# Optimization experiments

Hardware: AMD Instinct MI355X
Metric: run time of the kernel (lower is better)

Reference implementation:

```python
import jax, jax.numpy as jnp
import numpy as np

B, N, OUTERDIM, DIM, N_CLASSES = 2, 6000, 1024, 512, 2
HEADS, DIM_HEAD, INNER = 8, 64, 512
LANDMARKS, PINV_ITERS, KPAD = 256, 6, 16  # residual conv kernel 33 -> pad 16
SCALE = DIM_HEAD ** -0.5


def layer_norm(x, g, b, eps=1e-5):
    mu = x.mean(-1, keepdims=True)
    var = jnp.var(x, axis=-1, keepdims=True)
    return (x - mu) * jax.lax.rsqrt(var + eps) * g + b


def moore_penrose_pinv(x, iters=PINV_ITERS):
    # x: [b, h, m, m]
    abs_x = jnp.abs(x)
    col = abs_x.sum(-1)
    row = abs_x.sum(-2)
    z = jnp.swapaxes(x, -1, -2) / (jnp.max(col) * jnp.max(row))
    I = jnp.eye(x.shape[-1], dtype=x.dtype)
    for _ in range(iters):
        xz = x @ z
        z = 0.25 * z @ (13 * I - xz @ (15 * I - xz @ (7 * I - xz)))
    return z


def nystrom_attention(x, w_qkv, w_out, b_out, conv_w):
    b, n, _ = x.shape
    pad = (-n) % LANDMARKS
    xp = jnp.pad(x, ((0, 0), (pad, 0), (0, 0)))  # pad at FRONT, as in lucidrains impl
    npad = n + pad
    qkv = xp @ w_qkv.T  # [b, npad, 3*inner]
    q, k, v = [t.reshape(b, npad, HEADS, DIM_HEAD).transpose(0, 2, 1, 3)
               for t in jnp.split(qkv, 3, axis=-1)]
    q = q * SCALE
    l = npad // LANDMARKS  # tokens per landmark
    q_l = q.reshape(b, HEADS, LANDMARKS, l, DIM_HEAD).sum(3) / l
    k_l = k.reshape(b, HEADS, LANDMARKS, l, DIM_HEAD).sum(3) / l
    attn1 = jax.nn.softmax(jnp.einsum('bhid,bhjd->bhij', q, k_l), axis=-1)   # [b,h,npad,m]
    attn2 = jax.nn.softmax(jnp.einsum('bhid,bhjd->bhij', q_l, k_l), axis=-1)  # [b,h,m,m]
    attn3 = jax.nn.softmax(jnp.einsum('bhid,bhjd->bhij', q_l, k), axis=-1)    # [b,h,m,npad]
    out = (attn1 @ moore_penrose_pinv(attn2)) @ (attn3 @ v)  # [b,h,npad,d]
    # depthwise residual conv over sequence dim (per head), kernel (33,1)
    out = out + jax.lax.conv_general_dilated(
        v, conv_w, window_strides=(1, 1), padding=((KPAD, KPAD), (0, 0)),
        dimension_numbers=('NCHW', 'OIHW', 'NCHW'), feature_group_count=HEADS)
    out = out.transpose(0, 2, 1, 3).reshape(b, npad, INNER)
    out = out @ w_out.T + b_out
    return out[:, -n:]


def setup_inputs() -> dict:
    key = jax.random.key(0)
    ks = jax.random.split(key, 12)
    w = lambda k, shape: 0.02 * jax.random.normal(k, shape, dtype=jnp.float32)
    inp = {
        'data': jax.random.normal(ks[0], (B, N, OUTERDIM), dtype=jnp.float32),
        'w1': w(ks[1], (DIM, OUTERDIM)), 'b1': jnp.zeros((DIM,), jnp.float32),
        'cls_token': jax.random.normal(ks[2], (1, 1, DIM), dtype=jnp.float32),
        'ln1_g': jnp.ones((DIM,), jnp.float32), 'ln1_b': jnp.zeros((DIM,), jnp.float32),
        'qkv1_w': w(ks[3], (3 * INNER, DIM)),
        'out1_w': w(ks[4], (DIM, INNER)), 'out1_b': jnp.zeros((DIM,), jnp.float32),
        'conv1_w': w(ks[5], (HEADS, 1, 33, 1)),
        'ln2_g': jnp.ones((DIM,), jnp.float32), 'ln2_b': jnp.zeros((DIM,), jnp.float32),
        'qkv2_w': w(ks[6], (3 * INNER, DIM)),
        'out2_w': w(ks[7], (DIM, INNER)), 'out2_b': jnp.zeros((DIM,), jnp.float32),
        'conv2_w': w(ks[8], (HEADS, 1, 33, 1)),
        'lnf_g': jnp.ones((DIM,), jnp.float32), 'lnf_b': jnp.zeros((DIM,), jnp.float32),
        'w2': w(ks[9], (N_CLASSES, DIM)), 'b2': jnp.zeros((N_CLASSES,), jnp.float32),
    }
    return inp


def reference(data, w1, b1, cls_token, ln1_g, ln1_b, qkv1_w, out1_w, out1_b, conv1_w,
              ln2_g, ln2_b, qkv2_w, out2_w, out2_b, conv2_w, lnf_g, lnf_b, w2, b2):
    h = jax.nn.relu(data @ w1.T + b1)  # [B, N, DIM]
    H = h.shape[1]
    side = int(np.ceil(np.sqrt(H)))
    add = side * side - H
    h = jnp.concatenate([h, h[:, :add]], axis=1)  # square padding: 6084
    cls = jnp.broadcast_to(cls_token, (h.shape[0], 1, h.shape[2]))
    h = jnp.concatenate([cls, h], axis=1)  # +CLS: 6085
    h = h + nystrom_attention(layer_norm(h, ln1_g, ln1_b), qkv1_w, out1_w, out1_b, conv1_w)
    h = h + nystrom_attention(layer_norm(h, ln2_g, ln2_b), qkv2_w, out2_w, out2_b, conv2_w)
    h = layer_norm(h, lnf_g, lnf_b)[:, 0]
    logits = h @ w2.T + b2
    return logits
```

## Files before the change

### kernel.cpp

```cpp
#include <hip/hip_runtime.h>
#include <cstdint>
#include <cstddef>

namespace {

constexpr int DIMC  = 512;
constexpr int SEQ   = 6085;
constexpr int NPAD  = 6144;
constexpr int PADF  = 59;
constexpr int LMK   = 256;
constexpr int BHN   = 16;
constexpr int KSPL  = 16;
constexpr int MPADR = 6016;

typedef __attribute__((ext_vector_type(8))) short bf8_t;
typedef __attribute__((ext_vector_type(4))) float f4_t;

#define MFMA(a, b, c) __builtin_amdgcn_mfma_f32_16x16x32_bf16(a, b, c, 0, 0, 0)

#define SWZB(r, cu) (((((r) << 6) + ((cu) << 1))) ^ (((r) & 7) << 4))

#define GLDS16(gp, lp) __builtin_amdgcn_global_load_lds( \
    (const __attribute__((address_space(1))) void*)(gp), \
    (__attribute__((address_space(3))) void*)(lp), 16, 0, 0)

__device__ __forceinline__ ushort f2bf(float f) {
    union { float f; uint32_t u; } c{f};
    uint32_t u = c.u;
    return (ushort)((u + 0x7FFFu + ((u >> 16) & 1u)) >> 16);
}
__device__ __forceinline__ float bf2f(ushort u) {
    union { uint32_t u; float f; } c{(uint32_t)u << 16};
    return c.f;
}

__device__ __forceinline__ float waveSum(float v) {
#pragma unroll
    for (int o = 32; o > 0; o >>= 1) v += __shfl_xor(v, o, 64);
    return v;
}
__device__ __forceinline__ float waveMax(float v) {
#pragma unroll
    for (int o = 32; o > 0; o >>= 1) v = fmaxf(v, __shfl_xor(v, o, 64));
    return v;
}
__device__ __forceinline__ float blockSum256(float v, float* sm) {
    v = waveSum(v);
    __syncthreads();
    if ((threadIdx.x & 63) == 0) sm[threadIdx.x >> 6] = v;
    __syncthreads();
    return sm[0] + sm[1] + sm[2] + sm[3];
}
__device__ __forceinline__ float blockMax256(float v, float* sm) {
    v = waveMax(v);
    __syncthreads();
    if ((threadIdx.x & 63) == 0) sm[threadIdx.x >> 6] = v;
    __syncthreads();
    return fmaxf(fmaxf(sm[0], sm[1]), fmaxf(sm[2], sm[3]));
}
__device__ __forceinline__ float grpMax(float v) {
    v = fmaxf(v, __shfl_xor(v, 1, 64));
    v = fmaxf(v, __shfl_xor(v, 2, 64));
    v = fmaxf(v, __shfl_xor(v, 4, 64));
    v = fmaxf(v, __shfl_xor(v, 8, 64));
    return v;
}
__device__ __forceinline__ float grpSum(float v) {
    v += __shfl_xor(v, 1, 64);
    v += __shfl_xor(v, 2, 64);
    v += __shfl_xor(v, 4, 64);
    v += __shfl_xor(v, 8, 64);
    return v;
}

template<int EPI>
__global__ __launch_bounds__(256)
void gemm_bt(const ushort* __restrict__ A, const ushort* __restrict__ B,
             void* __restrict__ Cv, int M, int N, int K,
             int lda, int ldb, int ldc,
             long long sA, long long sB, long long sC,
             const float* __restrict__ bias, int relu,
             ushort* __restrict__ qp, ushort* __restrict__ kp, ushort* __restrict__ vp)
{
    __shared__ __align__(16) char As_s[128 * 128];
    __shared__ __align__(16) char Bs_s[128 * 128];
    const int gx = gridDim.x, gy = gridDim.y;
    const int total = gx * gy * gridDim.z;
    int flat = (blockIdx.z * gy + blockIdx.y) * gx + blockIdx.x;
    {
        int q = total >> 3, r = total & 7;
        int xcd = flat & 7, idx = flat >> 3;
        flat = (xcd < r ? xcd * (q + 1) : r * (q + 1) + (xcd - r) * q) + idx;
    }
    const int z = flat / (gx * gy);
    const int rem = flat - z * gx * gy;
    const int by = rem / gx, bx = rem - by * gx;

    const ushort* Ab = A + (size_t)z * sA;
    const ushort* Bb = B + (size_t)z * sB;
    const int row0 = by * 128, col0 = bx * 128;
    const int tid = threadIdx.x, wid = tid >> 6, lane = tid & 63;
    const int wr = wid >> 1, wc = wid & 1, lr = lane & 15, kg = lane >> 4;
    const int srow = lane >> 3, sq = lane & 7;
    f4_t acc[4][4] = {};
    for (int k0 = 0; k0 < K; k0 += 64) {
        __syncthreads();
#pragma unroll
        for (int i = 0; i < 4; ++i) {
            int r = wid * 32 + i * 8 + srow;
            int qs = sq ^ (r & 7);
            GLDS16(Ab + (size_t)(row0 + r) * lda + k0 + qs * 8,
                   As_s + (wid * 32 + i * 8) * 128);
        }
#pragma unroll
        for (int i = 0; i < 4; ++i) {
            int r = wid * 32 + i * 8 + srow;
            int qs = sq ^ (r & 7);
            GLDS16(Bb + (size_t)(col0 + r) * ldb + k0 + qs * 8,
                   Bs_s + (wid * 32 + i * 8) * 128);
        }
        asm volatile("s_waitcnt vmcnt(0)" ::: "memory");
        __syncthreads();
#pragma unroll
        for (int ks = 0; ks < 2; ++ks) {
            bf8_t af[4], bg[4];
#pragma unroll
            for (int mr = 0; mr < 4; ++mr) {
                int r = wr * 64 + mr * 16 + lr;
                af[mr] = *(const bf8_t*)(As_s + r * 128 + ((((ks << 2) | kg) ^ (r & 7)) << 4));
            }
#pragma unroll
            for (int nr = 0; nr < 4; ++nr) {
                int r = wc * 64 + nr * 16 + lr;
                bg[nr] = *(const bf8_t*)(Bs_s + r * 128 + ((((ks << 2) | kg) ^ (r & 7)) << 4));
            }
#pragma unroll
            for (int mr = 0; mr < 4; ++mr)
#pragma unroll
                for (int nr = 0; nr < 4; ++nr)
                    acc[mr][nr] = MFMA(af[mr], bg[nr], acc[mr][nr]);
        }
    }
#pragma unroll
    for (int mr = 0; mr < 4; ++mr) {
#pragma unroll
        for (int nr = 0; nr < 4; ++nr) {
#pragma unroll
            for (int r = 0; r < 4; ++r) {
                int gm = row0 + wr * 64 + mr * 16 + kg * 4 + r;
                int gn = col0 + wc * 64 + nr * 16 + lr;
                if (gm >= M || gn >= N) continue;
                float val = acc[mr][nr][r];
                if (EPI == 0) {
                    if (bias) val += bias[gn];
                    if (relu) val = fmaxf(val, 0.f);
                    ((float*)Cv)[(size_t)z * sC + (size_t)gm * ldc + gn] = val;
                } else if (EPI == 1) {
                    ((ushort*)Cv)[(size_t)z * sC + (size_t)gm * ldc + gn] = f2bf(val);
                } else {
                    int b = (gm >= NPAD) ? 1 : 0;
                    int i = gm - b * NPAD;
                    int which = gn >> 9, hh = (gn >> 6) & 7, d = gn & 63;
                    int bh = b * 8 + hh;
                    if (which == 0)
                        qp[((size_t)bh * NPAD + i) * 64 + d] = f2bf(val * 0.125f);
                    else if (which == 1)
                        kp[((size_t)bh * NPAD + i) * 64 + d] = f2bf(val);
                    else
                        vp[((size_t)bh * NPAD + i) * 64 + d] = f2bf(val);
                }
            }
        }
    }
}

template<int OC, int OCT, int CTD>
__global__ __launch_bounds__(256)
void gemm_nt(const ushort* __restrict__ A, const ushort* __restrict__ Bt,
             ushort* __restrict__ C, ushort* __restrict__ CT,
             float alpha, float cd, int K, int ldC, int ldCT,
             long long sA, long long sBt, long long sC, long long sCT)
{
    __shared__ __align__(16) char As_s[64 * 64];
    __shared__ __align__(16) char Bs_s[64 * 64];
    const int z = blockIdx.z;
    const int row0 = blockIdx.y * 64, col0 = blockIdx.x * 64;
    const int tid = threadIdx.x, wid = tid >> 6, lane = tid & 63;
    const int lr = lane & 15, kg = lane >> 4;
    const ushort* Ab = A + (size_t)z * sA;
    const ushort* Bb = Bt + (size_t)z * sBt;
    const int sr = tid >> 2, sc = (tid & 3) * 8;
    f4_t acc[4] = {};
    for (int k0 = 0; k0 < K; k0 += 32) {
        *(bf8_t*)(As_s + SWZB(sr, sc)) = *(const bf8_t*)&Ab[(size_t)(row0 + sr) * K + k0 + sc];
        *(bf8_t*)(Bs_s + SWZB(sr, sc)) = *(const bf8_t*)&Bb[(size_t)(col0 + sr) * K + k0 + sc];
        __syncthreads();
        bf8_t af = *(const bf8_t*)(As_s + SWZB(wid * 16 + lr, kg * 8));
#pragma unroll
        for (int j = 0; j < 4; ++j) {
            bf8_t bg = *(const bf8_t*)(Bs_s + SWZB(j * 16 + lr, kg * 8));
            acc[j] = MFMA(af, bg, acc[j]);
        }
        __syncthreads();
    }
#pragma unroll
    for (int j = 0; j < 4; ++j) {
#pragma unroll
        for (int r = 0; r < 4; ++r) {
            int gm = row0 + wid * 16 + kg * 4 + r;
            int gn = col0 + j * 16 + lr;
            float val = alpha * acc[j][r];
            if (OC) C[(size_t)z * sC + (size_t)gm * ldC + gn] = f2bf(val);
            if (OCT) CT[(size_t)z * sCT + (size_t)gn * ldCT + gm] =
                f2bf(CTD ? (((gm == gn) ? cd : 0.f) - val) : val);
        }
    }
}

__global__ __launch_bounds__(256)
void pv_splitk(const ushort* __restrict__ S, const ushort* __restrict__ v,
               float* __restrict__ o2p)
{
    __shared__ __align__(16) char As_s[128 * 64];
    __shared__ __align__(16) char Bs_s[64 * 64];
    const int split = blockIdx.x, mt = blockIdx.y, bh = blockIdx.z;
    const int tid = threadIdx.x;
    const int wid = tid >> 6, lane = tid & 63;
    const int lr = lane & 15, kg = lane >> 4;
    const ushort* Sb = S + (size_t)bh * LMK * NPAD + (size_t)(mt * 128) * NPAD;
    const ushort* vb = v + (size_t)bh * NPAD * 64;
    const int ks0 = split * (NPAD / KSPL);
    f4_t acc[2][4] = {};
    for (int k0 = ks0; k0 < ks0 + NPAD / KSPL; k0 += 32) {
#pragma unroll
        for (int p = 0; p < 2; ++p) {
            int idx = p * 256 + tid;
            int m = idx >> 2, kc = (idx & 3) * 8;
            *(bf8_t*)(As_s + SWZB(m, kc)) = *(const bf8_t*)&Sb[(size_t)m * NPAD + k0 + kc];
        }
#pragma unroll
        for (int p = 0; p < 8; ++p) {
            int kk = p * 4 + (tid >> 6), n = tid & 63;
            *(ushort*)(Bs_s + SWZB(n, kk)) = vb[(size_t)(k0 + kk) * 64 + n];
        }
        __syncthreads();
        bf8_t af[2], bg[4];
#pragma unroll
        for (int i = 0; i < 2; ++i)
            af[i] = *(const bf8_t*)(As_s + SWZB(wid * 32 + i * 16 + lr, kg * 8));
#pragma unroll
        for (int j = 0; j < 4; ++j)
            bg[j] = *(const bf8_t*)(Bs_s + SWZB(j * 16 + lr, kg * 8));
#pragma unroll
        for (int i = 0; i < 2; ++i)
#pragma unroll
            for (int j = 0; j < 4; ++j)
                acc[i][j] = MFMA(af[i], bg[j], acc[i][j]);
        __syncthreads();
    }
#pragma unroll
    for (int i = 0; i < 2; ++i)
#pragma unroll
        for (int j = 0; j < 4; ++j)
#pragma unroll
            for (int r = 0; r < 4; ++r) {
                int gm = mt * 128 + wid * 32 + i * 16 + kg * 4 + r;
                int gn = j * 16 + lr;
                o2p[((size_t)(split * BHN + bh) * LMK + gm) * 64 + gn] = acc[i][j][r];
            }
}

__global__ void reduce_o2(const float* __restrict__ o2p, ushort* __restrict__ o2t) {
    int idx = blockIdx.x * 256 + threadIdx.x;
    int bh = idx >> 14, m = (idx >> 6) & 255, d = idx & 63;
    float s = 0.f;
#pragma unroll
    for (int sp = 0; sp < KSPL; ++sp)
        s += o2p[((size_t)(sp * BHN + bh) << 14) + (m << 6) + d];
    o2t[((size_t)bh * 64 + d) * 256 + m] = f2bf(s);
}

__global__ __launch_bounds__(256)
void attn1_fused(const ushort* __restrict__ q, const ushort* __restrict__ kl,
                 const ushort* __restrict__ Wt, ushort* __restrict__ ot)
{
    __shared__ __align__(16) char P_s[64 * 512];
    const int mt = blockIdx.x;
    const int bh = blockIdx.y;
    const int b = bh >> 3, hh = bh & 7;
    const int tid = threadIdx.x, wid = tid >> 6, lane = tid & 63;
    const int lr = lane & 15, kg = lane >> 4;
    const int row0 = mt * 64, rowb = wid * 16;
    const ushort* qb  = q  + (size_t)bh * NPAD * 64;
    const ushort* klb = kl + (size_t)bh * LMK * 64;
    const ushort* Wtb = Wt + (size_t)bh * 128 * 256;

    f4_t acc[16];
#pragma unroll
    for (int nf = 0; nf < 16; ++nf) acc[nf] = (f4_t){0.f, 0.f, 0.f, 0.f};
#pragma unroll
    for (int ks = 0; ks < 2; ++ks) {
        bf8_t af = *(const bf8_t*)&qb[(size_t)(row0 + rowb + lr) * 64 + ks * 32 + kg * 8];
#pragma unroll
        for (int nf = 0; nf < 16; ++nf) {
            bf8_t bg = *(const bf8_t*)&klb[(size_t)(nf * 16 + lr) * 64 + ks * 32 + kg * 8];
            acc[nf] = MFMA(af, bg, acc[nf]);
        }
    }
    float inv_s[4];
    {
        float mx[4] = {-3.0e38f, -3.0e38f, -3.0e38f, -3.0e38f};
#pragma unroll
        for (int nf = 0; nf < 16; ++nf)
#pragma unroll
            for (int r = 0; r < 4; ++r) mx[r] = fmaxf(mx[r], acc[nf][r]);
#pragma unroll
        for (int r = 0; r < 4; ++r) mx[r] = grpMax(mx[r]);
        float sum[4] = {0.f, 0.f, 0.f, 0.f};
        const int rb2 = rowb + kg * 4;
        const int cc2 = (lr & 7) * 2, chi = lr >> 3;
#pragma unroll
        for (int nf = 0; nf < 16; ++nf)
#pragma unroll
            for (int r = 0; r < 4; ++r) {
                float e = __expf(acc[nf][r] - mx[r]);
                sum[r] += e;
                int row = rb2 + r;
                int chunk = (2 * nf + chi) ^ (row & 7);
                *(ushort*)(P_s + row * 512 + chunk * 16 + cc2) = f2bf(e);
            }
#pragma unroll
        for (int r = 0; r < 4; ++r) inv_s[r] = 1.f / grpSum(sum[r]);
    }
    f4_t acc2[4] = {};
#pragma unroll
    for (int kt = 0; kt < 8; ++kt) {
        int row = rowb + lr;
        int chunk = (kt * 4 + kg) ^ (row & 7);
        bf8_t af2 = *(const bf8_t*)(P_s + row * 512 + chunk * 16);
#pragma unroll
        for (int nf = 0; nf < 4; ++nf) {
            bf8_t bg = *(const bf8_t*)&Wtb[(size_t)(nf * 16 + lr) * 256 + kt * 32 + kg * 8];
            acc2[nf] = MFMA(af2, bg, acc2[nf]);
        }
    }
#pragma unroll
    for (int nf = 0; nf < 4; ++nf)
#pragma unroll
        for (int r = 0; r < 4; ++r) {
            int gm = row0 + rowb + kg * 4 + r;
            int gn = nf * 16 + lr;
            ot[((size_t)(b * NPAD + gm)) * DIMC + hh * 64 + gn] = f2bf(acc2[nf][r] * inv_s[r]);
        }
}

__global__ void cvt_bf16(const float* __restrict__ in, ushort* __restrict__ out, int n8) {
    int i = blockIdx.x * 256 + threadIdx.x;
    if (i >= n8) return;
    float4 a = ((const float4*)in)[i * 2], b = ((const float4*)in)[i * 2 + 1];
    ushort4 lo = { f2bf(a.x), f2bf(a.y), f2bf(a.z), f2bf(a.w) };
    ushort4 hi = { f2bf(b.x), f2bf(b.y), f2bf(b.z), f2bf(b.w) };
    ((ushort4*)out)[i * 2] = lo;
    ((ushort4*)out)[i * 2 + 1] = hi;
}

__global__ void extend_h(float* __restrict__ h, const float* __restrict__ cls) {
    int b = blockIdx.y, bx = blockIdx.x;
    float* hb = h + (size_t)b * SEQ * DIMC;
    for (int c = threadIdx.x; c < DIMC; c += 256) {
        if (bx == 0) hb[c] = cls[c];
        else hb[(size_t)(6000 + bx) * DIMC + c] = hb[(size_t)bx * DIMC + c];
    }
}

__global__ void zero_xp_pad(ushort* __restrict__ xp) {
    int e = blockIdx.x * 256 + threadIdx.x;
    int b = e / (PADF * DIMC);
    int rest = e - b * (PADF * DIMC);
    xp[(size_t)b * NPAD * DIMC + rest] = 0;
}

__global__ __launch_bounds__(128)
void ln_to_xp(const float* __restrict__ h, const float* __restrict__ g,
              const float* __restrict__ bb, ushort* __restrict__ xp)
{
    __shared__ float sm[2];
    int r = blockIdx.x;
    int b = r / SEQ, i = r - b * SEQ;
    int t = threadIdx.x;
    const float4* row = (const float4*)(h + (size_t)r * DIMC);
    float4 x = row[t];
    float s  = x.x + x.y + x.z + x.w;
    float sq = x.x * x.x + x.y * x.y + x.z * x.z + x.w * x.w;
    s = waveSum(s);
    sq = waveSum(sq);
    int w = t >> 6;
    if ((t & 63) == 0) sm[w] = s;
    __syncthreads();
    float S = sm[0] + sm[1];
    __syncthreads();
    if ((t & 63) == 0) sm[w] = sq;
    __syncthreads();
    float SQ = sm[0] + sm[1];
    float mu = S * (1.f / DIMC);
    float var = SQ * (1.f / DIMC) - mu * mu;
    float rs = rsqrtf(var + 1e-5f);
    float4 gg = ((const float4*)g)[t];
    float4 bv = ((const float4*)bb)[t];
    ushort4 o;
    o.x = f2bf((x.x - mu) * rs * gg.x + bv.x);
    o.y = f2bf((x.y - mu) * rs * gg.y + bv.y);
    o.z = f2bf((x.z - mu) * rs * gg.z + bv.z);
    o.w = f2bf((x.w - mu) * rs * gg.w + bv.w);
    ((ushort4*)(xp + ((size_t)b * NPAD + PADF + i) * DIMC))[t] = o;
}

__global__ void landmark_mean(const ushort* __restrict__ in, ushort* __restrict__ out) {
    int m = blockIdx.x, bh = blockIdx.y, d = threadIdx.x;
    const ushort* p = in + ((size_t)bh * NPAD + (size_t)m * (NPAD / LMK)) * 64 + d;
    float s = 0.f;
#pragma unroll
    for (int j = 0; j < NPAD / LMK; ++j) s += bf2f(p[(size_t)j * 64]);
    out[((size_t)bh * LMK + m) * 64 + d] = f2bf(s * (1.f / (NPAD / LMK)));
}

__global__ __launch_bounds__(256)
void softmax_bf_wide(ushort* __restrict__ S) {
    __shared__ float sm[4];
    ushort* p = S + (size_t)blockIdx.x * NPAD;
    int t = threadIdx.x;
    float v[24];
    float mx = -1e30f;
#pragma unroll
    for (int j = 0; j < 24; ++j) { v[j] = bf2f(p[j * 256 + t]); mx = fmaxf(mx, v[j]); }
    float bm = blockMax256(mx, sm);
    float s = 0.f;
#pragma unroll
    for (int j = 0; j < 24; ++j) { v[j] = __expf(v[j] - bm); s += v[j]; }
    float bs = blockSum256(s, sm);
    float inv = 1.f / bs;
#pragma unroll
    for (int j = 0; j < 24; ++j) p[j * 256 + t] = f2bf(v[j] * inv);
}

__global__ __launch_bounds__(256)
void softmax_bf256(ushort* __restrict__ S) {
    __shared__ float sm[4];
    ushort* p = S + (size_t)blockIdx.x * 256;
    int t = threadIdx.x;
    float v = bf2f(p[t]);
    float bm = blockMax256(v, sm);
    float e = __expf(v - bm);
    float bs = blockSum256(e, sm);
    p[t] = f2bf(e / bs);
}

__global__ __launch_bounds__(256)
void colsum_max(const ushort* __restrict__ X, float* __restrict__ scal) {
    __shared__ float sm[4];
    int bh = blockIdx.x, t = threadIdx.x;
    const ushort* Xb = X + ((size_t)bh << 16);
    float s = 0.f;
#pragma unroll 8
    for (int i = 0; i < 256; ++i) s += bf2f(Xb[(size_t)i * 256 + t]);
    float m = blockMax256(s, sm);
    if (t == 0) atomicMax((unsigned int*)scal, __float_as_uint(m));
}

__global__ void init_z(const ushort* __restrict__ X, const float* __restrict__ scal,
                       ushort* __restrict__ Z, ushort* __restrict__ Zt) {
    size_t e = (size_t)blockIdx.x * 256 + threadIdx.x;
    int c = (int)(e & 255);
    int r = (int)((e >> 8) & 255);
    size_t bh = e >> 16;
    float inv = 1.f / scal[0];
    Z[e]  = f2bf(bf2f(X[(bh << 16) + (size_t)c * 256 + r]) * inv);
    Zt[e] = f2bf(bf2f(X[e]) * inv);
}

__global__ __launch_bounds__(256)
void conv_add(const ushort* __restrict__ v, const float* __restrict__ cw,
              ushort* __restrict__ ot)
{
    __shared__ float w[33];
    __shared__ ushort vt[96][64];
    int bh = blockIdx.y;
    int b = bh >> 3, hh = bh & 7;
    int i0 = blockIdx.x * 64;
    int t = threadIdx.x;
    if (t < 33) w[t] = cw[hh * 33 + t];
    const ushort* vb = v + (size_t)bh * NPAD * 64;
    int d = t & 63;
    for (int rr = t >> 6; rr < 96; rr += 4) {
        int j = i0 - 16 + rr;
        vt[rr][d] = (j >= 0 && j < NPAD) ? vb[(size_t)j * 64 + d] : (ushort)0;
    }
    __syncthreads();
    for (int ii = t >> 6; ii < 64; ii += 4) {
        float acc = 0.f;
#pragma unroll
        for (int kk = 0; kk < 33; ++kk) acc += w[kk] * bf2f(vt[ii + kk][d]);
        size_t off = ((size_t)(b * NPAD + i0 + ii)) * DIMC + hh * 64 + d;
        ot[off] = f2bf(bf2f(ot[off]) + acc);
    }
}

__global__ void residual_add(float* __restrict__ h, const float* __restrict__ y) {
    size_t e = (size_t)blockIdx.x * 256 + threadIdx.x;
    int c = (int)(e & 511);
    size_t ri = e >> 9;
    int i = (int)(ri % SEQ);
    int b = (int)(ri / SEQ);
    h[e] += y[((size_t)b * NPAD + PADF + i) * DIMC + c];
}

__global__ __launch_bounds__(256)
void final_head(const float* __restrict__ h, const float* __restrict__ g,
                const float* __restrict__ bb, const float* __restrict__ w2,
                const float* __restrict__ b2, float* __restrict__ out)
{
    __shared__ float row[DIMC];
    __shared__ float sm[4];
    int b = blockIdx.x;
    int t = threadIdx.x;
    const float* x = h + (size_t)b * SEQ * DIMC;
    float v0 = x[t], v1 = x[t + 256];
    float S = blockSum256(v0 + v1, sm);
    float SQ = blockSum256(v0 * v0 + v1 * v1, sm);
    float mu = S * (1.f / DIMC);
    float rs = rsqrtf(SQ * (1.f / DIMC) - mu * mu + 1e-5f);
    row[t] = (v0 - mu) * rs * g[t] + bb[t];
    row[t + 256] = (v1 - mu) * rs * g[t + 256] + bb[t + 256];
    __syncthreads();
    if (t < 64) {
        float a0 = 0.f, a1 = 0.f;
        for (int idx = t; idx < DIMC; idx += 64) {
            a0 += row[idx] * w2[idx];
            a1 += row[idx] * w2[DIMC + idx];
        }
        a0 = waveSum(a0);
        a1 = waveSum(a1);
        if (t == 0) {
            out[b * 2 + 0] = a0 + b2[0];
            out[b * 2 + 1] = a1 + b2[1];
        }
    }
}

void bt(int epi, const ushort* A, const ushort* B, void* C, int M, int N, int K,
        int lda, int ldb, int ldc, long long sA, long long sB, long long sC, int batch,
        const float* bias, int relu, ushort* qp, ushort* kp, ushort* vp, hipStream_t s)
{
    dim3 g((N + 127) / 128, (M + 127) / 128, batch), blk(256);
    switch (epi) {
    case 0: gemm_bt<0><<<g, blk, 0, s>>>(A, B, C, M, N, K, lda, ldb, ldc, sA, sB, sC, bias, relu, qp, kp, vp); break;
    case 1: gemm_bt<1><<<g, blk, 0, s>>>(A, B, C, M, N, K, lda, ldb, ldc, sA, sB, sC, bias, relu, qp, kp, vp); break;
    default: gemm_bt<2><<<g, blk, 0, s>>>(A, B, C, M, N, K, lda, ldb, ldc, sA, sB, sC, bias, relu, qp, kp, vp); break;
    }
}

void nt(int mode, const ushort* A, const ushort* Bt, ushort* C, ushort* CT,
        float alpha, float cd, int M, int N, int K, int ldC, int ldCT,
        long long sA, long long sBt, long long sC, long long sCT, hipStream_t s)
{
    dim3 g(N / 64, M / 64, BHN), blk(256);
    switch (mode) {
    case 0: gemm_nt<1, 1, 1><<<g, blk, 0, s>>>(A, Bt, C, CT, alpha, cd, K, ldC, ldCT, sA, sBt, sC, sCT); break;
    case 1: gemm_nt<0, 1, 1><<<g, blk, 0, s>>>(A, Bt, C, CT, alpha, cd, K, ldC, ldCT, sA, sBt, sC, sCT); break;
    case 2: gemm_nt<1, 1, 0><<<g, blk, 0, s>>>(A, Bt, C, CT, alpha, cd, K, ldC, ldCT, sA, sBt, sC, sCT); break;
    default: gemm_nt<0, 1, 0><<<g, blk, 0, s>>>(A, Bt, C, CT, alpha, cd, K, ldC, ldCT, sA, sBt, sC, sCT); break;
    }
}

struct WS {
    float *h, *scal, *o2p, *y;
    ushort *xp, *q, *k, *v, *ql, *kl;
    ushort *datab, *w1b, *qkvwb1, *qkvwb2, *outwb1, *outwb2;
    ushort *X, *Y, *TAt, *TBt, *Z0, *Z0t, *Z1, *Z1t;
    ushort *o2t, *Wt, *S, *ot;
};

void nystrom_layer(float* h, const float* lng, const float* lnb,
                   const ushort* qkvwb, const ushort* outwb, const float* outb,
                   const float* convw, const WS& w, hipStream_t s)
{
    const long long SM = (long long)LMK * LMK;
    zero_xp_pad<<<(2 * PADF * DIMC) / 256, 256, 0, s>>>(w.xp);
    ln_to_xp<<<2 * SEQ, 128, 0, s>>>(h, lng, lnb, w.xp);
    bt(2, w.xp, qkvwb, nullptr, 2 * NPAD, 3 * DIMC, DIMC, DIMC, DIMC, 0,
       0, 0, 0, 1, nullptr, 0, w.q, w.k, w.v, s);
    landmark_mean<<<dim3(LMK, BHN), 64, 0, s>>>(w.q, w.ql);
    landmark_mean<<<dim3(LMK, BHN), 64, 0, s>>>(w.k, w.kl);
    bt(1, w.ql, w.kl, w.X, LMK, LMK, 64, 64, 64, LMK,
       (long long)LMK * 64, (long long)LMK * 64, SM, BHN,
       nullptr, 0, nullptr, nullptr, nullptr, s);
    softmax_bf256<<<BHN * LMK, 256, 0, s>>>(w.X);
    hipMemsetAsync(w.scal, 0, 8, s);
    colsum_max<<<BHN, 256, 0, s>>>(w.X, w.scal);
    init_z<<<(BHN * LMK * LMK) / 256, 256, 0, s>>>(w.X, w.scal, w.Z0, w.Z0t);
    ushort *Zc = w.Z0, *Zct = w.Z0t, *Zn = w.Z1, *Znt = w.Z1t;
    for (int it = 0; it < 6; ++it) {
        nt(0, w.X, Zct, w.Y, w.TAt, 1.f, 7.f, LMK, LMK, LMK, 256, 256, SM, SM, SM, SM, s);
        nt(1, w.Y, w.TAt, nullptr, w.TBt, 1.f, 15.f, LMK, LMK, LMK, 256, 256, SM, SM, 0, SM, s);
        nt(1, w.Y, w.TBt, nullptr, w.TAt, 1.f, 13.f, LMK, LMK, LMK, 256, 256, SM, SM, 0, SM, s);
        nt(2, Zc, w.TAt, Zn, Znt, 0.25f, 0.f, LMK, LMK, LMK, 256, 256, SM, SM, SM, SM, s);
        ushort* t;
        t = Zc; Zc = Zn; Zn = t;
        t = Zct; Zct = Znt; Znt = t;
    }
    bt(1, w.ql, w.k, w.S, LMK, NPAD, 64, 64, 64, NPAD,
       (long long)LMK * 64, (long long)NPAD * 64, (long long)LMK * NPAD, BHN,
       nullptr, 0, nullptr, nullptr, nullptr, s);
    softmax_bf_wide<<<BHN * LMK, 256, 0, s>>>(w.S);
    pv_splitk<<<dim3(KSPL, 2, BHN), 256, 0, s>>>(w.S, w.v, w.o2p);
    reduce_o2<<<BHN * LMK * 64 / 256, 256, 0, s>>>(w.o2p, w.o2t);
    nt(3, Zc, w.o2t, nullptr, w.Wt, 1.f, 0.f, LMK, 64, LMK, 256, 256,
       SM, 64 * 256, 0, 128 * 256, s);
    attn1_fused<<<dim3(NPAD / 64, BHN), 256, 0, s>>>(w.q, w.kl, w.Wt, w.ot);
    conv_add<<<dim3(NPAD / 64, BHN), 256, 0, s>>>(w.v, convw, w.ot);
    bt(0, w.ot, outwb, w.y, 2 * NPAD, DIMC, DIMC, DIMC, DIMC, DIMC,
       0, 0, 0, 1, outb, 0, nullptr, nullptr, nullptr, s);
    residual_add<<<(2 * SEQ * DIMC) / 256, 256, 0, s>>>(h, w.y);
}

}

extern "C" void kernel_launch(void* const* d_in, const int* in_sizes, int n_in,
                              void* d_out, int out_size, void* d_ws, size_t ws_size,
                              hipStream_t stream)
{
    (void)in_sizes; (void)n_in; (void)out_size;
    const float* data  = (const float*)d_in[0];
    const float* w1    = (const float*)d_in[1];
    const float* b1    = (const float*)d_in[2];
    const float* cls   = (const float*)d_in[3];
    const float* ln1g  = (const float*)d_in[4];
    const float* ln1b  = (const float*)d_in[5];
    const float* qkv1w = (const float*)d_in[6];
    const float* out1w = (const float*)d_in[7];
    const float* out1b = (const float*)d_in[8];
    const float* conv1 = (const float*)d_in[9];
    const float* ln2g  = (const float*)d_in[10];
    const float* ln2b  = (const float*)d_in[11];
    const float* qkv2w = (const float*)d_in[12];
    const float* out2w = (const float*)d_in[13];
    const float* out2b = (const float*)d_in[14];
    const float* conv2 = (const float*)d_in[15];
    const float* lnfg  = (const float*)d_in[16];
    const float* lnfb  = (const float*)d_in[17];
    const float* w2    = (const float*)d_in[18];
    const float* b2    = (const float*)d_in[19];
    float* out = (float*)d_out;

    if (ws_size < 209473792ull) return;
    char* p = (char*)d_ws;
    auto alloc = [&](size_t bytes) { char* r = p; p += (bytes + 255) & ~(size_t)255; return r; };
    WS w;
    w.h     = (float*)alloc((size_t)2 * SEQ * DIMC * 4);
    w.xp    = (ushort*)alloc((size_t)2 * NPAD * DIMC * 2);
    w.q     = (ushort*)alloc((size_t)BHN * NPAD * 64 * 2);
    w.k     = (ushort*)alloc((size_t)BHN * NPAD * 64 * 2);
    w.v     = (ushort*)alloc((size_t)BHN * NPAD * 64 * 2);
    w.ql    = (ushort*)alloc((size_t)BHN * LMK * 64 * 2);
    w.kl    = (ushort*)alloc((size_t)BHN * LMK * 64 * 2);
    w.scal  = (float*)alloc(256);
    w.datab = (ushort*)alloc((size_t)2 * MPADR * 1024 * 2);
    w.w1b   = (ushort*)alloc((size_t)512 * 1024 * 2);
    w.qkvwb1= (ushort*)alloc((size_t)1536 * 512 * 2);
    w.qkvwb2= (ushort*)alloc((size_t)1536 * 512 * 2);
    w.outwb1= (ushort*)alloc((size_t)512 * 512 * 2);
    w.outwb2= (ushort*)alloc((size_t)512 * 512 * 2);
    w.X     = (ushort*)alloc((size_t)BHN * LMK * LMK * 2);
    w.Y     = (ushort*)alloc((size_t)BHN * LMK * LMK * 2);
    w.TAt   = (ushort*)alloc((size_t)BHN * LMK * LMK * 2);
    w.TBt   = (ushort*)alloc((size_t)BHN * LMK * LMK * 2);
    w.Z0    = (ushort*)alloc((size_t)BHN * LMK * LMK * 2);
    w.Z0t   = (ushort*)alloc((size_t)BHN * LMK * LMK * 2);
    w.Z1    = (ushort*)alloc((size_t)BHN * LMK * LMK * 2);
    w.Z1t   = (ushort*)alloc((size_t)BHN * LMK * LMK * 2);
    w.o2p   = (float*)alloc((size_t)KSPL * BHN * LMK * 64 * 4);
    w.o2t   = (ushort*)alloc((size_t)BHN * 64 * 256 * 2);
    w.Wt    = (ushort*)alloc((size_t)BHN * 128 * 256 * 2);
    w.S     = (ushort*)alloc((size_t)BHN * LMK * NPAD * 2);
    w.y     = (float*)w.S;
    w.ot    = w.k;

    for (int b = 0; b < 2; ++b)
        cvt_bf16<<<3000, 256, 0, stream>>>(data + (size_t)b * 6000 * 1024,
                                           w.datab + (size_t)b * MPADR * 1024, 768000);
    cvt_bf16<<<256, 256, 0, stream>>>(w1, w.w1b, 65536);
    cvt_bf16<<<384, 256, 0, stream>>>(qkv1w, w.qkvwb1, 98304);
    cvt_bf16<<<384, 256, 0, stream>>>(qkv2w, w.qkvwb2, 98304);
    cvt_bf16<<<128, 256, 0, stream>>>(out1w, w.outwb1, 32768);
    cvt_bf16<<<128, 256, 0, stream>>>(out2w, w.outwb2, 32768);

    bt(0, w.datab, w.w1b, w.h + DIMC, 6000, DIMC, 1024, 1024, 1024, DIMC,
       (long long)MPADR * 1024, 0, (long long)SEQ * DIMC, 2, b1, 1,
       nullptr, nullptr, nullptr, stream);
    extend_h<<<dim3(85, 2), 256, 0, stream>>>(w.h, cls);

    nystrom_layer(w.h, ln1g, ln1b, w.qkvwb1, w.outwb1, out1b, conv1, w, stream);
    nystrom_layer(w.h, ln2g, ln2b, w.qkvwb2, w.outwb2, out2b, conv2, w, stream);

    final_head<<<2, 256, 0, stream>>>(w.h, lnfg, lnfb, w2, b2, out);
}
```

Measured before the change: 961.1 us.

## Emit transposed V from QKV epilogue and stage full-K tiles in pinv GEMM

The QKV GEMM epilogue now also writes a transposed copy of V. This lets pv_splitk load its B tile with 16-byte vector loads instead of 2-byte strided scalar loads. The small 256x256 pinv GEMM (gemm_nt) now loads the whole K=256 slab of A and B into swizzled LDS once, using global_load_lds, and drops the per-k-step loop and its barriers. The costs are extra scattered 2-byte stores for vT, a larger workspace that the unchanged size check does not account for, 64KB of LDS per block, and a K of 256 that is now hardcoded.

```diff
diff --git a/kernel.cpp b/kernel.cpp
--- a/kernel.cpp
+++ b/kernel.cpp
@@ -80,7 +80,8 @@
              int lda, int ldb, int ldc,
              long long sA, long long sB, long long sC,
              const float* __restrict__ bias, int relu,
-             ushort* __restrict__ qp, ushort* __restrict__ kp, ushort* __restrict__ vp)
+             ushort* __restrict__ qp, ushort* __restrict__ kp,
+             ushort* __restrict__ vp, ushort* __restrict__ vtp)
 {
     __shared__ __align__(16) char As_s[128 * 128];
     __shared__ __align__(16) char Bs_s[128 * 128];
@@ -166,8 +167,11 @@
                         qp[((size_t)bh * NPAD + i) * 64 + d] = f2bf(val * 0.125f);
                     else if (which == 1)
                         kp[((size_t)bh * NPAD + i) * 64 + d] = f2bf(val);
-                    else
-                        vp[((size_t)bh * NPAD + i) * 64 + d] = f2bf(val);
+                    else {
+                        ushort bv = f2bf(val);
+                        vp[((size_t)bh * NPAD + i) * 64 + d] = bv;
+                        vtp[((size_t)bh * 64 + d) * NPAD + i] = bv;
+                    }
                 }
             }
         }
@@ -178,30 +182,46 @@
 __global__ __launch_bounds__(256)
 void gemm_nt(const ushort* __restrict__ A, const ushort* __restrict__ Bt,
              ushort* __restrict__ C, ushort* __restrict__ CT,
-             float alpha, float cd, int K, int ldC, int ldCT,
+             float alpha, float cd, int ldC, int ldCT,
              long long sA, long long sBt, long long sC, long long sCT)
 {
-    __shared__ __align__(16) char As_s[64 * 64];
-    __shared__ __align__(16) char Bs_s[64 * 64];
+    __shared__ __align__(16) char As_s[64 * 512];
+    __shared__ __align__(16) char Bs_s[64 * 512];
     const int z = blockIdx.z;
     const int row0 = blockIdx.y * 64, col0 = blockIdx.x * 64;
     const int tid = threadIdx.x, wid = tid >> 6, lane = tid & 63;
     const int lr = lane & 15, kg = lane >> 4;
     const ushort* Ab = A + (size_t)z * sA;
     const ushort* Bb = Bt + (size_t)z * sBt;
-    const int sr = tid >> 2, sc = (tid & 3) * 8;
+    const int srow8 = lane >> 5;
+    const int sch = lane & 31;
+#pragma unroll
+    for (int i = 0; i < 8; ++i) {
+        int rb = i * 8 + wid * 2 + srow8;
+        int qs = sch ^ (rb & 7);
+        GLDS16(Ab + (size_t)(row0 + rb) * 256 + qs * 8,
+               As_s + (i * 8 + wid * 2) * 512);
+    }
+#pragma unroll
+    for (int i = 0; i < 8; ++i) {
+        int rb = i * 8 + wid * 2 + srow8;
+        int qs = sch ^ (rb & 7);
+        GLDS16(Bb + (size_t)(col0 + rb) * 256 + qs * 8,
+               Bs_s + (i * 8 + wid * 2) * 512);
+    }
+    asm volatile("s_waitcnt vmcnt(0)" ::: "memory");
+    __syncthreads();
     f4_t acc[4] = {};
-    for (int k0 = 0; k0 < K; k0 += 32) {
-        *(bf8_t*)(As_s + SWZB(sr, sc)) = *(const bf8_t*)&Ab[(size_t)(row0 + sr) * K + k0 + sc];
-        *(bf8_t*)(Bs_s + SWZB(sr, sc)) = *(const bf8_t*)&Bb[(size_t)(col0 + sr) * K + k0 + sc];
-        __syncthreads();
-        bf8_t af = *(const bf8_t*)(As_s + SWZB(wid * 16 + lr, kg * 8));
+    const int arow = wid * 16 + lr;
+#pragma unroll
+    for (int ks = 0; ks < 8; ++ks) {
+        bf8_t af = *(const bf8_t*)(As_s + arow * 512 + (((ks * 4 + kg) ^ (arow & 7)) << 4));
 #pragma unroll
         for (int j = 0; j < 4; ++j) {
-            bf8_t bg = *(const bf8_t*)(Bs_s + SWZB(j * 16 + lr, kg * 8));
+            int brow = j * 16 + lr;
+            bf8_t bg = *(const bf8_t*)(Bs_s + brow * 512 + (((ks * 4 + kg) ^ (brow & 7)) << 4));
             acc[j] = MFMA(af, bg, acc[j]);
         }
-        __syncthreads();
     }
 #pragma unroll
     for (int j = 0; j < 4; ++j) {
@@ -218,7 +238,7 @@
 }
 
 __global__ __launch_bounds__(256)
-void pv_splitk(const ushort* __restrict__ S, const ushort* __restrict__ v,
+void pv_splitk(const ushort* __restrict__ S, const ushort* __restrict__ vT,
                float* __restrict__ o2p)
 {
     __shared__ __align__(16) char As_s[128 * 64];
@@ -228,7 +248,7 @@
     const int wid = tid >> 6, lane = tid & 63;
     const int lr = lane & 15, kg = lane >> 4;
     const ushort* Sb = S + (size_t)bh * LMK * NPAD + (size_t)(mt * 128) * NPAD;
-    const ushort* vb = v + (size_t)bh * NPAD * 64;
+    const ushort* vTb = vT + (size_t)bh * 64 * NPAD;
     const int ks0 = split * (NPAD / KSPL);
     f4_t acc[2][4] = {};
     for (int k0 = ks0; k0 < ks0 + NPAD / KSPL; k0 += 32) {
@@ -238,10 +258,9 @@
             int m = idx >> 2, kc = (idx & 3) * 8;
             *(bf8_t*)(As_s + SWZB(m, kc)) = *(const bf8_t*)&Sb[(size_t)m * NPAD + k0 + kc];
         }
-#pragma unroll
-        for (int p = 0; p < 8; ++p) {
-            int kk = p * 4 + (tid >> 6), n = tid & 63;
-            *(ushort*)(Bs_s + SWZB(n, kk)) = vb[(size_t)(k0 + kk) * 64 + n];
+        {
+            int n = tid >> 2, kc = (tid & 3) * 8;
+            *(bf8_t*)(Bs_s + SWZB(n, kc)) = *(const bf8_t*)&vTb[(size_t)n * NPAD + k0 + kc];
         }
         __syncthreads();
         bf8_t af[2], bg[4];
@@ -549,32 +568,33 @@
 
 void bt(int epi, const ushort* A, const ushort* B, void* C, int M, int N, int K,
         int lda, int ldb, int ldc, long long sA, long long sB, long long sC, int batch,
-        const float* bias, int relu, ushort* qp, ushort* kp, ushort* vp, hipStream_t s)
+        const float* bias, int relu, ushort* qp, ushort* kp, ushort* vp, ushort* vtp,
+        hipStream_t s)
 {
     dim3 g((N + 127) / 128, (M + 127) / 128, batch), blk(256);
     switch (epi) {
-    case 0: gemm_bt<0><<<g, blk, 0, s>>>(A, B, C, M, N, K, lda, ldb, ldc, sA, sB, sC, bias, relu, qp, kp, vp); break;
-    case 1: gemm_bt<1><<<g, blk, 0, s>>>(A, B, C, M, N, K, lda, ldb, ldc, sA, sB, sC, bias, relu, qp, kp, vp); break;
-    default: gemm_bt<2><<<g, blk, 0, s>>>(A, B, C, M, N, K, lda, ldb, ldc, sA, sB, sC, bias, relu, qp, kp, vp); break;
+    case 0: gemm_bt<0><<<g, blk, 0, s>>>(A, B, C, M, N, K, lda, ldb, ldc, sA, sB, sC, bias, relu, qp, kp, vp, vtp); break;
+    case 1: gemm_bt<1><<<g, blk, 0, s>>>(A, B, C, M, N, K, lda, ldb, ldc, sA, sB, sC, bias, relu, qp, kp, vp, vtp); break;
+    default: gemm_bt<2><<<g, blk, 0, s>>>(A, B, C, M, N, K, lda, ldb, ldc, sA, sB, sC, bias, relu, qp, kp, vp, vtp); break;
     }
 }
 
 void nt(int mode, const ushort* A, const ushort* Bt, ushort* C, ushort* CT,
-        float alpha, float cd, int M, int N, int K, int ldC, int ldCT,
+        float alpha, float cd, int M, int N, int ldC, int ldCT,
         long long sA, long long sBt, long long sC, long long sCT, hipStream_t s)
 {
     dim3 g(N / 64, M / 64, BHN), blk(256);
     switch (mode) {
-    case 0: gemm_nt<1, 1, 1><<<g, blk, 0, s>>>(A, Bt, C, CT, alpha, cd, K, ldC, ldCT, sA, sBt, sC, sCT); break;
-    case 1: gemm_nt<0, 1, 1><<<g, blk, 0, s>>>(A, Bt, C, CT, alpha, cd, K, ldC, ldCT, sA, sBt, sC, sCT); break;
-    case 2: gemm_nt<1, 1, 0><<<g, blk, 0, s>>>(A, Bt, C, CT, alpha, cd, K, ldC, ldCT, sA, sBt, sC, sCT); break;
-    default: gemm_nt<0, 1, 0><<<g, blk, 0, s>>>(A, Bt, C, CT, alpha, cd, K, ldC, ldCT, sA, sBt, sC, sCT); break;
+    case 0: gemm_nt<1, 1, 1><<<g, blk, 0, s>>>(A, Bt, C, CT, alpha, cd, ldC, ldCT, sA, sBt, sC, sCT); break;
+    case 1: gemm_nt<0, 1, 1><<<g, blk, 0, s>>>(A, Bt, C, CT, alpha, cd, ldC, ldCT, sA, sBt, sC, sCT); break;
+    case 2: gemm_nt<1, 1, 0><<<g, blk, 0, s>>>(A, Bt, C, CT, alpha, cd, ldC, ldCT, sA, sBt, sC, sCT); break;
+    default: gemm_nt<0, 1, 0><<<g, blk, 0, s>>>(A, Bt, C, CT, alpha, cd, ldC, ldCT, sA, sBt, sC, sCT); break;
     }
 }
 
 struct WS {
     float *h, *scal, *o2p, *y;
-    ushort *xp, *q, *k, *v, *ql, *kl;
+    ushort *xp, *q, *k, *v, *vT, *ql, *kl;
     ushort *datab, *w1b, *qkvwb1, *qkvwb2, *outwb1, *outwb2;
     ushort *X, *Y, *TAt, *TBt, *Z0, *Z0t, *Z1, *Z1t;
     ushort *o2t, *Wt, *S, *ot;
@@ -588,38 +608,38 @@
     zero_xp_pad<<<(2 * PADF * DIMC) / 256, 256, 0, s>>>(w.xp);
     ln_to_xp<<<2 * SEQ, 128, 0, s>>>(h, lng, lnb, w.xp);
     bt(2, w.xp, qkvwb, nullptr, 2 * NPAD, 3 * DIMC, DIMC, DIMC, DIMC, 0,
-       0, 0, 0, 1, nullptr, 0, w.q, w.k, w.v, s);
+       0, 0, 0, 1, nullptr, 0, w.q, w.k, w.v, w.vT, s);
     landmark_mean<<<dim3(LMK, BHN), 64, 0, s>>>(w.q, w.ql);
     landmark_mean<<<dim3(LMK, BHN), 64, 0, s>>>(w.k, w.kl);
     bt(1, w.ql, w.kl, w.X, LMK, LMK, 64, 64, 64, LMK,
        (long long)LMK * 64, (long long)LMK * 64, SM, BHN,
-       nullptr, 0, nullptr, nullptr, nullptr, s);
+       nullptr, 0, nullptr, nullptr, nullptr, nullptr, s);
     softmax_bf256<<<BHN * LMK, 256, 0, s>>>(w.X);
     hipMemsetAsync(w.scal, 0, 8, s);
     colsum_max<<<BHN, 256, 0, s>>>(w.X, w.scal);
     init_z<<<(BHN * LMK * LMK) / 256, 256, 0, s>>>(w.X, w.scal, w.Z0, w.Z0t);
     ushort *Zc = w.Z0, *Zct = w.Z0t, *Zn = w.Z1, *Znt = w.Z1t;
     for (int it = 0; it < 6; ++it) {
-        nt(0, w.X, Zct, w.Y, w.TAt, 1.f, 7.f, LMK, LMK, LMK, 256, 256, SM, SM, SM, SM, s);
-        nt(1, w.Y, w.TAt, nullptr, w.TBt, 1.f, 15.f, LMK, LMK, LMK, 256, 256, SM, SM, 0, SM, s);
-        nt(1, w.Y, w.TBt, nullptr, w.TAt, 1.f, 13.f, LMK, LMK, LMK, 256, 256, SM, SM, 0, SM, s);
-        nt(2, Zc, w.TAt, Zn, Znt, 0.25f, 0.f, LMK, LMK, LMK, 256, 256, SM, SM, SM, SM, s);
+        nt(0, w.X, Zct, w.Y, w.TAt, 1.f, 7.f, LMK, LMK, 256, 256, SM, SM, SM, SM, s);
+        nt(1, w.Y, w.TAt, nullptr, w.TBt, 1.f, 15.f, LMK, LMK, 256, 256, SM, SM, 0, SM, s);
+        nt(1, w.Y, w.TBt, nullptr, w.TAt, 1.f, 13.f, LMK, LMK, 256, 256, SM, SM, 0, SM, s);
+        nt(2, Zc, w.TAt, Zn, Znt, 0.25f, 0.f, LMK, LMK, 256, 256, SM, SM, SM, SM, s);
         ushort* t;
         t = Zc; Zc = Zn; Zn = t;
         t = Zct; Zct = Znt; Znt = t;
     }
     bt(1, w.ql, w.k, w.S, LMK, NPAD, 64, 64, 64, NPAD,
        (long long)LMK * 64, (long long)NPAD * 64, (long long)LMK * NPAD, BHN,
-       nullptr, 0, nullptr, nullptr, nullptr, s);
+       nullptr, 0, nullptr, nullptr, nullptr, nullptr, s);
     softmax_bf_wide<<<BHN * LMK, 256, 0, s>>>(w.S);
-    pv_splitk<<<dim3(KSPL, 2, BHN), 256, 0, s>>>(w.S, w.v, w.o2p);
+    pv_splitk<<<dim3(KSPL, 2, BHN), 256, 0, s>>>(w.S, w.vT, w.o2p);
     reduce_o2<<<BHN * LMK * 64 / 256, 256, 0, s>>>(w.o2p, w.o2t);
-    nt(3, Zc, w.o2t, nullptr, w.Wt, 1.f, 0.f, LMK, 64, LMK, 256, 256,
+    nt(3, Zc, w.o2t, nullptr, w.Wt, 1.f, 0.f, LMK, 64, 256, 256,
        SM, 64 * 256, 0, 128 * 256, s);
     attn1_fused<<<dim3(NPAD / 64, BHN), 256, 0, s>>>(w.q, w.kl, w.Wt, w.ot);
     conv_add<<<dim3(NPAD / 64, BHN), 256, 0, s>>>(w.v, convw, w.ot);
     bt(0, w.ot, outwb, w.y, 2 * NPAD, DIMC, DIMC, DIMC, DIMC, DIMC,
-       0, 0, 0, 1, outb, 0, nullptr, nullptr, nullptr, s);
+       0, 0, 0, 1, outb, 0, nullptr, nullptr, nullptr, nullptr, s);
     residual_add<<<(2 * SEQ * DIMC) / 256, 256, 0, s>>>(h, w.y);
 }
 
@@ -661,6 +681,7 @@
     w.q     = (ushort*)alloc((size_t)BHN * NPAD * 64 * 2);
     w.k     = (ushort*)alloc((size_t)BHN * NPAD * 64 * 2);
     w.v     = (ushort*)alloc((size_t)BHN * NPAD * 64 * 2);
+    w.vT    = (ushort*)alloc((size_t)BHN * 64 * NPAD * 2);
     w.ql    = (ushort*)alloc((size_t)BHN * LMK * 64 * 2);
     w.kl    = (ushort*)alloc((size_t)BHN * LMK * 64 * 2);
     w.scal  = (float*)alloc(256);
@@ -696,7 +717,7 @@
 
     bt(0, w.datab, w.w1b, w.h + DIMC, 6000, DIMC, 1024, 1024, 1024, DIMC,
        (long long)MPADR * 1024, 0, (long long)SEQ * DIMC, 2, b1, 1,
-       nullptr, nullptr, nullptr, stream);
+       nullptr, nullptr, nullptr, nullptr, stream);
     extend_h<<<dim3(85, 2), 256, 0, stream>>>(w.h, cls);
 
     nystrom_layer(w.h, ln1g, ln1b, w.qkvwb1, w.outwb1, out1b, conv1, w, stream);
```

Result: faster. 896.5 us (-6.7%).
